# Kernel optimization log

Hardware: AMD Instinct MI355X
Metric: run time of the kernel (lower is better)

The kernel has to match this reference:

```python
import jax, jax.numpy as jnp
import numpy as np

B, T, D, H, C, WIN = 2, 2048, 512, 8, 64, 128
EPS = 1e-6


def _rms_norm(x, w):
    # x: (..., C)
    norm = jax.lax.rsqrt(jnp.mean(x * x, axis=-1, keepdims=True) + EPS)
    return x * norm * w


def _apply_rope(x, cos_p, sin_p):
    # x: (B, H, T, C); cos_p/sin_p: (T, C)
    half = x.shape[-1] // 2
    x1, x2 = x[..., :half], x[..., half:]
    rotated = jnp.concatenate([-x2, x1], axis=-1)
    return x * cos_p + rotated * sin_p


def setup_inputs() -> dict:
    key = jax.random.key(0)
    ks = jax.random.split(key, 5)
    h = jax.random.normal(ks[0], (B, T, D), dtype=jnp.float32)
    # RoPE cache (rotate-half convention): (T_max, head_dim)
    inv_freq = 1.0 / (10000.0 ** (jnp.arange(0, C, 2, dtype=jnp.float32) / C))  # (C/2,)
    pos = jnp.arange(T, dtype=jnp.float32)
    freqs = pos[:, None] * inv_freq[None, :]                      # (T, C/2)
    emb = jnp.concatenate([freqs, freqs], axis=-1)                # (T, C)
    rope_cos = jnp.cos(emb)
    rope_sin = jnp.sin(emb)
    scale = 0.02
    W_q = jax.random.normal(ks[1], (D, H * C), dtype=jnp.float32) * scale
    W_k = jax.random.normal(ks[2], (D, H * C), dtype=jnp.float32) * scale
    W_v = jax.random.normal(ks[3], (D, H * C), dtype=jnp.float32) * scale
    W_o = jax.random.normal(ks[4], (H * C, D), dtype=jnp.float32) * scale
    q_norm_w = jnp.ones((C,), dtype=jnp.float32)
    k_norm_w = jnp.ones((C,), dtype=jnp.float32)
    return {"h": h, "rope_cos": rope_cos, "rope_sin": rope_sin,
            "W_q": W_q, "W_k": W_k, "W_v": W_v, "W_o": W_o,
            "q_norm_w": q_norm_w, "k_norm_w": k_norm_w}


def reference(h, rope_cos, rope_sin, W_q, W_k, W_v, W_o, q_norm_w, k_norm_w):
    Bx, Tx, _ = h.shape
    q = (h @ W_q).reshape(Bx, Tx, H, C)
    k = (h @ W_k).reshape(Bx, Tx, H, C)
    v = (h @ W_v).reshape(Bx, Tx, H, C)
    q = _rms_norm(q, q_norm_w)
    k = _rms_norm(k, k_norm_w)
    positions = jnp.arange(Tx)
    cos_p = rope_cos[positions]   # (T, C)
    sin_p = rope_sin[positions]
    # transpose to (B, H, T, C), apply rope, transpose back handled implicitly
    q = _apply_rope(q.transpose(0, 2, 1, 3), cos_p, sin_p).transpose(0, 2, 1, 3)
    k = _apply_rope(k.transpose(0, 2, 1, 3), cos_p, sin_p).transpose(0, 2, 1, 3)
    i = positions[:, None]
    j = positions[None, :]
    sw_mask = (j <= i) & (j > i - WIN)                # (T, T) banded causal
    logits = jnp.einsum('bthc,bshc->bhts', q, k) / np.sqrt(C).astype(np.float32)
    logits = jnp.where(sw_mask[None, None], logits, jnp.float32(-jnp.inf))
    attn = jax.nn.softmax(logits, axis=-1)
    out = jnp.einsum('bhts,bshc->bthc', attn, v).reshape(Bx, Tx, H * C)
    return out @ W_o
```

## Files before the change

kernel.cpp:

```cpp
#include <hip/hip_runtime.h>
#include <hip/hip_bf16.h>
#include <cmath>

#define Bb 2
#define Tt 2048
#define Dd 512
#define Hh 8
#define Cc 64
#define WINw 128

using u16x8 = __attribute__((ext_vector_type(8))) unsigned short;
using s16x8 = __attribute__((ext_vector_type(8))) short;
using f32x4 = __attribute__((ext_vector_type(4))) float;

__device__ __forceinline__ float bf2f(unsigned short u) {
  union { unsigned int i; float f; } v; v.i = ((unsigned int)u) << 16; return v.f;
}
__device__ __forceinline__ unsigned short f2bf(float f) {
  __hip_bfloat16 b = __float2bfloat16(f);
  return *reinterpret_cast<unsigned short*>(&b);
}

__global__ __launch_bounds__(256) void cvt_f32_bf16(
    const float* __restrict__ src, unsigned short* __restrict__ dst) {
  size_t i = ((size_t)blockIdx.x * 256 + threadIdx.x) * 8;
  const float4* g = (const float4*)&src[i];
  float4 f0 = g[0], f1 = g[1];
  u16x8 o = {f2bf(f0.x), f2bf(f0.y), f2bf(f0.z), f2bf(f0.w),
             f2bf(f1.x), f2bf(f1.y), f2bf(f1.z), f2bf(f1.w)};
  *(u16x8*)&dst[i] = o;
}

__global__ __launch_bounds__(256) void transpose_all(
    const float* __restrict__ s0, const float* __restrict__ s1,
    const float* __restrict__ s2, const float* __restrict__ s3,
    unsigned short* __restrict__ d) {
  __shared__ unsigned short tile[64 * 65];
  const float* srcs[4] = {s0, s1, s2, s3};
  const float* src = srcs[blockIdx.z];
  unsigned short* dst = d + (size_t)blockIdx.z * 512 * 512;
  int n0 = blockIdx.x * 64, k0 = blockIdx.y * 64;
  int tx = threadIdx.x, ty = threadIdx.y;
  #pragma unroll
  for (int i = 0; i < 16; ++i) {
    int k = ty * 16 + i;
    tile[k * 65 + tx] = f2bf(src[(k0 + k) * 512 + n0 + tx]);
  }
  __syncthreads();
  #pragma unroll
  for (int i = 0; i < 16; ++i) {
    int n = ty * 16 + i;
    dst[(n0 + n) * 512 + k0 + tx] = tile[tx * 65 + n];
  }
}

__global__ __launch_bounds__(256) void qkv_fused(
    const unsigned short* __restrict__ Hb,
    const unsigned short* __restrict__ WTall,
    const float* __restrict__ qnw, const float* __restrict__ knw,
    const float* __restrict__ rcos, const float* __restrict__ rsin,
    unsigned short* __restrict__ Qw, unsigned short* __restrict__ Kw,
    unsigned short* __restrict__ Vw) {
  __shared__ alignas(16) unsigned short Al[128 * 72];
  __shared__ alignas(16) unsigned short Bl[128 * 72];
  int m0 = blockIdx.x * 128;
  int n0 = blockIdx.y * 128;
  int tid = threadIdx.x;
  int wave = tid >> 6, lane = tid & 63;
  int ln = lane & 15, qd = lane >> 4;
  int wm = wave >> 1, wn = wave & 1;
  int srow = tid >> 2, scol = (tid & 3) * 16;

  f32x4 acc[4][4];
  #pragma unroll
  for (int mi = 0; mi < 4; ++mi)
    #pragma unroll
    for (int ni = 0; ni < 4; ++ni) acc[mi][ni] = f32x4{0.f, 0.f, 0.f, 0.f};

  for (int k0 = 0; k0 < 512; k0 += 64) {
    #pragma unroll
    for (int p = 0; p < 2; ++p) {
      int row = p * 64 + srow;
      const u16x8* ga = (const u16x8*)&Hb[(size_t)(m0 + row) * 512 + k0 + scol];
      u16x8 a0 = ga[0], a1 = ga[1];
      const u16x8* gb = (const u16x8*)&WTall[(size_t)(n0 + row) * 512 + k0 + scol];
      u16x8 b0 = gb[0], b1 = gb[1];
      *(u16x8*)&Al[row * 72 + scol] = a0;
      *(u16x8*)&Al[row * 72 + scol + 8] = a1;
      *(u16x8*)&Bl[row * 72 + scol] = b0;
      *(u16x8*)&Bl[row * 72 + scol + 8] = b1;
    }
    __syncthreads();
    #pragma unroll
    for (int kk = 0; kk < 64; kk += 32) {
      s16x8 af[4], bfr[4];
      #pragma unroll
      for (int mi = 0; mi < 4; ++mi)
        af[mi] = *(const s16x8*)&Al[(wm * 64 + mi * 16 + ln) * 72 + kk + qd * 8];
      #pragma unroll
      for (int ni = 0; ni < 4; ++ni)
        bfr[ni] = *(const s16x8*)&Bl[(wn * 64 + ni * 16 + ln) * 72 + kk + qd * 8];
      #pragma unroll
      for (int mi = 0; mi < 4; ++mi)
        #pragma unroll
        for (int ni = 0; ni < 4; ++ni)
          acc[mi][ni] = __builtin_amdgcn_mfma_f32_16x16x32_bf16(
              af[mi], bfr[ni], acc[mi][ni], 0, 0, 0);
    }
    __syncthreads();
  }

  int gh = blockIdx.y * 2 + wn;
  int mat = gh >> 3, head = gh & 7;
  unsigned short* Out = (mat == 0) ? Qw : (mat == 1) ? Kw : Vw;
  const float* nw = (mat == 0) ? qnw : knw;
  bool do_rope = (mat < 2);

  #pragma unroll
  for (int mi = 0; mi < 4; ++mi) {
    float vals[4][4];
    #pragma unroll
    for (int ni = 0; ni < 4; ++ni)
      #pragma unroll
      for (int r = 0; r < 4; ++r) vals[ni][r] = acc[mi][ni][r];

    if (do_rope) {
      #pragma unroll
      for (int r = 0; r < 4; ++r) {
        float ss = 0.f;
        #pragma unroll
        for (int ni = 0; ni < 4; ++ni) ss += vals[ni][r] * vals[ni][r];
        ss += __shfl_xor(ss, 1, 64);
        ss += __shfl_xor(ss, 2, 64);
        ss += __shfl_xor(ss, 4, 64);
        ss += __shfl_xor(ss, 8, 64);
        float nrm = rsqrtf(ss * (1.0f / 64.0f) + 1e-6f);
        #pragma unroll
        for (int ni = 0; ni < 4; ++ni) vals[ni][r] *= nrm;
      }
      #pragma unroll
      for (int ni = 0; ni < 4; ++ni) {
        float w = nw[ni * 16 + ln];
        #pragma unroll
        for (int r = 0; r < 4; ++r) vals[ni][r] *= w;
      }
      float res[4][4];
      #pragma unroll
      for (int r = 0; r < 4; ++r) {
        int row = m0 + wm * 64 + mi * 16 + qd * 4 + r;
        int t = row & (Tt - 1);
        #pragma unroll
        for (int ni = 0; ni < 4; ++ni) {
          int c = ni * 16 + ln;
          float cs = rcos[t * 64 + c];
          float sn = rsin[t * 64 + c];
          float part = vals[ni ^ 2][r];
          float rot = (ni < 2) ? -part : part;
          res[ni][r] = vals[ni][r] * cs + rot * sn;
        }
      }
      #pragma unroll
      for (int ni = 0; ni < 4; ++ni)
        #pragma unroll
        for (int r = 0; r < 4; ++r) vals[ni][r] = res[ni][r];
    }

    #pragma unroll
    for (int r = 0; r < 4; ++r) {
      int row = m0 + wm * 64 + mi * 16 + qd * 4 + r;
      int b = row >> 11, t = row & (Tt - 1);
      unsigned short* op = &Out[(((size_t)b * Hh + head) * Tt + t) * 64 + ln];
      #pragma unroll
      for (int ni = 0; ni < 4; ++ni) op[ni * 16] = f2bf(vals[ni][r]);
    }
  }
}

__global__ __launch_bounds__(256) void attn_mfma(
    const unsigned short* __restrict__ Q,
    const unsigned short* __restrict__ K,
    const unsigned short* __restrict__ V,
    unsigned short* __restrict__ AO) {
  __shared__ alignas(16) unsigned short Ql[64 * 72];
  __shared__ alignas(16) unsigned short KP[192 * 72];
  __shared__ alignas(16) unsigned short Vt[64 * 200];

  int tid = threadIdx.x;
  int wave = tid >> 6, lane = tid & 63;
  int ln = lane & 15, qd = lane >> 4;
  int qtile = blockIdx.x, bh = blockIdx.y;
  int t0 = qtile * 64;
  int kb = t0 - 128;

  const unsigned short* Qg = Q + ((size_t)bh * Tt + t0) * 64;
  const unsigned short* Kg = K + (size_t)bh * Tt * 64;
  const unsigned short* Vg = V + (size_t)bh * Tt * 64;

  int srow = tid >> 2;
  int scol = (tid & 3) * 16;

  {
    const u16x8* g = (const u16x8*)&Qg[srow * 64 + scol];
    u16x8 a0 = g[0], a1 = g[1];
    *(u16x8*)&Ql[srow * 72 + scol] = a0;
    *(u16x8*)&Ql[srow * 72 + scol + 8] = a1;
  }
  #pragma unroll
  for (int p = 0; p < 3; ++p) {
    int row = p * 64 + srow;
    int kg = kb + row; if (kg < 0) kg = 0;
    const u16x8* gk = (const u16x8*)&Kg[kg * 64 + scol];
    u16x8 k0 = gk[0], k1 = gk[1];
    const u16x8* gv = (const u16x8*)&Vg[kg * 64 + scol];
    u16x8 v0 = gv[0], v1 = gv[1];
    *(u16x8*)&KP[row * 72 + scol] = k0;
    *(u16x8*)&KP[row * 72 + scol + 8] = k1;
    #pragma unroll
    for (int j = 0; j < 8; ++j) {
      Vt[(scol + j) * 200 + row] = v0[j];
      Vt[(scol + 8 + j) * 200 + row] = v1[j];
    }
  }
  __syncthreads();

  int q0 = wave * 16;
  s16x8 aq0 = *(const s16x8*)&Ql[(q0 + ln) * 72 + qd * 8];
  s16x8 aq1 = *(const s16x8*)&Ql[(q0 + ln) * 72 + 32 + qd * 8];
  f32x4 sf[12];
  #pragma unroll
  for (int nt = 0; nt < 12; ++nt) {
    s16x8 b0 = *(const s16x8*)&KP[(nt * 16 + ln) * 72 + qd * 8];
    s16x8 b1 = *(const s16x8*)&KP[(nt * 16 + ln) * 72 + 32 + qd * 8];
    f32x4 acc = {0.f, 0.f, 0.f, 0.f};
    acc = __builtin_amdgcn_mfma_f32_16x16x32_bf16(aq0, b0, acc, 0, 0, 0);
    acc = __builtin_amdgcn_mfma_f32_16x16x32_bf16(aq1, b1, acc, 0, 0, 0);
    sf[nt] = acc;
  }
  __syncthreads();

  unsigned short* Pl = KP;
  int ok0 = (t0 < 128) ? (128 - t0) : 0;
  #pragma unroll
  for (int r = 0; r < 4; ++r) {
    int lq = q0 + qd * 4 + r;
    float mx = -INFINITY;
    #pragma unroll
    for (int nt = 0; nt < 12; ++nt) {
      int kk = nt * 16 + ln;
      bool valid = (kk > lq) && (kk <= lq + 128) && (kk >= ok0);
      float s = valid ? sf[nt][r] * 0.125f : -INFINITY;
      sf[nt][r] = s;
      mx = fmaxf(mx, s);
    }
    mx = fmaxf(mx, __shfl_xor(mx, 1, 64));
    mx = fmaxf(mx, __shfl_xor(mx, 2, 64));
    mx = fmaxf(mx, __shfl_xor(mx, 4, 64));
    mx = fmaxf(mx, __shfl_xor(mx, 8, 64));
    float sum = 0.f;
    #pragma unroll
    for (int nt = 0; nt < 12; ++nt) {
      float e = __expf(sf[nt][r] - mx);
      sf[nt][r] = e;
      sum += e;
    }
    sum += __shfl_xor(sum, 1, 64);
    sum += __shfl_xor(sum, 2, 64);
    sum += __shfl_xor(sum, 4, 64);
    sum += __shfl_xor(sum, 8, 64);
    float inv = 1.0f / sum;
    #pragma unroll
    for (int nt = 0; nt < 12; ++nt)
      Pl[lq * 200 + nt * 16 + ln] = f2bf(sf[nt][r] * inv);
  }
  __syncthreads();

  f32x4 oa[4] = {f32x4{0,0,0,0}, f32x4{0,0,0,0}, f32x4{0,0,0,0}, f32x4{0,0,0,0}};
  #pragma unroll
  for (int s = 0; s < 6; ++s) {
    s16x8 ap = *(const s16x8*)&Pl[(q0 + ln) * 200 + s * 32 + qd * 8];
    #pragma unroll
    for (int nt = 0; nt < 4; ++nt) {
      s16x8 bv = *(const s16x8*)&Vt[(nt * 16 + ln) * 200 + s * 32 + qd * 8];
      oa[nt] = __builtin_amdgcn_mfma_f32_16x16x32_bf16(ap, bv, oa[nt], 0, 0, 0);
    }
  }

  int b = bh >> 3, h = bh & 7;
  #pragma unroll
  for (int r = 0; r < 4; ++r) {
    int t = t0 + q0 + qd * 4 + r;
    unsigned short* op = &AO[(((size_t)b * Tt + t) * Hh + h) * 64 + ln];
    #pragma unroll
    for (int nt = 0; nt < 4; ++nt) op[nt * 16] = f2bf(oa[nt][r]);
  }
}

__global__ __launch_bounds__(256) void out_gemm128(
    const unsigned short* __restrict__ Am,
    const unsigned short* __restrict__ WT,
    float* __restrict__ Out) {
  __shared__ alignas(16) unsigned short Al[128 * 72];
  __shared__ alignas(16) unsigned short Bl[128 * 72];
  int m0 = blockIdx.x * 128;
  int n0 = blockIdx.y * 128;
  int tid = threadIdx.x;
  int wave = tid >> 6, lane = tid & 63;
  int ln = lane & 15, qd = lane >> 4;
  int wm = wave >> 1, wn = wave & 1;
  int srow = tid >> 2, scol = (tid & 3) * 16;

  f32x4 acc[4][4];
  #pragma unroll
  for (int mi = 0; mi < 4; ++mi)
    #pragma unroll
    for (int ni = 0; ni < 4; ++ni) acc[mi][ni] = f32x4{0.f, 0.f, 0.f, 0.f};

  for (int k0 = 0; k0 < 512; k0 += 64) {
    #pragma unroll
    for (int p = 0; p < 2; ++p) {
      int row = p * 64 + srow;
      const u16x8* ga = (const u16x8*)&Am[(size_t)(m0 + row) * 512 + k0 + scol];
      u16x8 a0 = ga[0], a1 = ga[1];
      const u16x8* gb = (const u16x8*)&WT[(size_t)(n0 + row) * 512 + k0 + scol];
      u16x8 b0 = gb[0], b1 = gb[1];
      *(u16x8*)&Al[row * 72 + scol] = a0;
      *(u16x8*)&Al[row * 72 + scol + 8] = a1;
      *(u16x8*)&Bl[row * 72 + scol] = b0;
      *(u16x8*)&Bl[row * 72 + scol + 8] = b1;
    }
    __syncthreads();
    #pragma unroll
    for (int kk = 0; kk < 64; kk += 32) {
      s16x8 af[4], bfr[4];
      #pragma unroll
      for (int mi = 0; mi < 4; ++mi)
        af[mi] = *(const s16x8*)&Al[(wm * 64 + mi * 16 + ln) * 72 + kk + qd * 8];
      #pragma unroll
      for (int ni = 0; ni < 4; ++ni)
        bfr[ni] = *(const s16x8*)&Bl[(wn * 64 + ni * 16 + ln) * 72 + kk + qd * 8];
      #pragma unroll
      for (int mi = 0; mi < 4; ++mi)
        #pragma unroll
        for (int ni = 0; ni < 4; ++ni)
          acc[mi][ni] = __builtin_amdgcn_mfma_f32_16x16x32_bf16(
              af[mi], bfr[ni], acc[mi][ni], 0, 0, 0);
    }
    __syncthreads();
  }

  #pragma unroll
  for (int mi = 0; mi < 4; ++mi)
    #pragma unroll
    for (int r = 0; r < 4; ++r) {
      int row = m0 + wm * 64 + mi * 16 + qd * 4 + r;
      #pragma unroll
      for (int ni = 0; ni < 4; ++ni)
        Out[(size_t)row * 512 + n0 + wn * 64 + ni * 16 + ln] = acc[mi][ni][r];
    }
}

extern "C" void kernel_launch(void* const* d_in, const int* in_sizes, int n_in,
                              void* d_out, int out_size, void* d_ws, size_t ws_size,
                              hipStream_t stream) {
  const float* h   = (const float*)d_in[0];
  const float* rc  = (const float*)d_in[1];
  const float* rs  = (const float*)d_in[2];
  const float* Wq  = (const float*)d_in[3];
  const float* Wk  = (const float*)d_in[4];
  const float* Wv  = (const float*)d_in[5];
  const float* Wo  = (const float*)d_in[6];
  const float* qnw = (const float*)d_in[7];
  const float* knw = (const float*)d_in[8];

  unsigned short* ws    = (unsigned short*)d_ws;
  unsigned short* WTall = ws;
  unsigned short* WTo   = WTall + 1536 * 512;
  unsigned short* Hb    = WTo + 512 * 512;
  unsigned short* Qw    = Hb + 2097152;
  unsigned short* Kw    = Qw + 2097152;
  unsigned short* Vw    = Kw + 2097152;
  unsigned short* AOw   = Vw + 2097152;

  cvt_f32_bf16<<<1024, 256, 0, stream>>>(h, Hb);
  transpose_all<<<dim3(8, 8, 4), dim3(64, 4), 0, stream>>>(Wq, Wk, Wv, Wo, WTall);

  qkv_fused<<<dim3(32, 12), 256, 0, stream>>>(Hb, WTall, qnw, knw, rc, rs,
                                              Qw, Kw, Vw);

  attn_mfma<<<dim3(32, 16), 256, 0, stream>>>(Qw, Kw, Vw, AOw);

  out_gemm128<<<dim3(32, 4), 256, 0, stream>>>(AOw, WTo, (float*)d_out);
}
```

Before: 116.9 us.

## Merge prep kernels, use direct global-to-LDS loads with XOR swizzle, shrink out-GEMM tile

Folds the h conversion and the weight transposes into one launch, removing a kernel launch. Both GEMMs now stage tiles through global_load_lds straight into an unpadded LDS layout, using an XOR swizzle to avoid bank conflicts, which skips the trip through registers. The output GEMM tile drops from 128 to 64 rows, doubling its block count to fill more CUs. In exchange, the conversion blocks do uneven work relative to the transpose blocks, and the smaller tile reuses less data per block.

```diff
diff --git a/kernel.cpp b/kernel.cpp
--- a/kernel.cpp
+++ b/kernel.cpp
@@ -21,26 +21,36 @@
   return *reinterpret_cast<unsigned short*>(&b);
 }
 
-__global__ __launch_bounds__(256) void cvt_f32_bf16(
-    const float* __restrict__ src, unsigned short* __restrict__ dst) {
-  size_t i = ((size_t)blockIdx.x * 256 + threadIdx.x) * 8;
-  const float4* g = (const float4*)&src[i];
-  float4 f0 = g[0], f1 = g[1];
-  u16x8 o = {f2bf(f0.x), f2bf(f0.y), f2bf(f0.z), f2bf(f0.w),
-             f2bf(f1.x), f2bf(f1.y), f2bf(f1.z), f2bf(f1.w)};
-  *(u16x8*)&dst[i] = o;
-}
-
-__global__ __launch_bounds__(256) void transpose_all(
+#define GLD16(gp, lp)                                                        \
+  __builtin_amdgcn_global_load_lds(                                          \
+      (const __attribute__((address_space(1))) unsigned int*)(gp),           \
+      (__attribute__((address_space(3))) unsigned int*)(lp), 16, 0, 0)
+
+__global__ __launch_bounds__(256) void prep_all(
     const float* __restrict__ s0, const float* __restrict__ s1,
     const float* __restrict__ s2, const float* __restrict__ s3,
-    unsigned short* __restrict__ d) {
+    unsigned short* __restrict__ d,
+    const float* __restrict__ hsrc, unsigned short* __restrict__ hdst) {
+  int tid = threadIdx.x;
+  if (blockIdx.z == 4) {
+    int gid = ((int)blockIdx.y * 8 + blockIdx.x) * 256 + tid;
+    #pragma unroll
+    for (int s = 0; s < 16; ++s) {
+      size_t i = ((size_t)s * 16384 + gid) * 8;
+      const float4* g = (const float4*)&hsrc[i];
+      float4 f0 = g[0], f1 = g[1];
+      u16x8 o = {f2bf(f0.x), f2bf(f0.y), f2bf(f0.z), f2bf(f0.w),
+                 f2bf(f1.x), f2bf(f1.y), f2bf(f1.z), f2bf(f1.w)};
+      *(u16x8*)&hdst[i] = o;
+    }
+    return;
+  }
   __shared__ unsigned short tile[64 * 65];
   const float* srcs[4] = {s0, s1, s2, s3};
   const float* src = srcs[blockIdx.z];
   unsigned short* dst = d + (size_t)blockIdx.z * 512 * 512;
   int n0 = blockIdx.x * 64, k0 = blockIdx.y * 64;
-  int tx = threadIdx.x, ty = threadIdx.y;
+  int tx = tid & 63, ty = tid >> 6;
   #pragma unroll
   for (int i = 0; i < 16; ++i) {
     int k = ty * 16 + i;
@@ -61,15 +71,13 @@
     const float* __restrict__ rcos, const float* __restrict__ rsin,
     unsigned short* __restrict__ Qw, unsigned short* __restrict__ Kw,
     unsigned short* __restrict__ Vw) {
-  __shared__ alignas(16) unsigned short Al[128 * 72];
-  __shared__ alignas(16) unsigned short Bl[128 * 72];
-  int m0 = blockIdx.x * 128;
-  int n0 = blockIdx.y * 128;
+  __shared__ alignas(16) unsigned short Al[128 * 64];
+  __shared__ alignas(16) unsigned short Bl[128 * 64];
   int tid = threadIdx.x;
   int wave = tid >> 6, lane = tid & 63;
   int ln = lane & 15, qd = lane >> 4;
   int wm = wave >> 1, wn = wave & 1;
-  int srow = tid >> 2, scol = (tid & 3) * 16;
+  int m0 = blockIdx.x * 128, n0 = blockIdx.y * 128;
 
   f32x4 acc[4][4];
   #pragma unroll
@@ -79,27 +87,32 @@
 
   for (int k0 = 0; k0 < 512; k0 += 64) {
     #pragma unroll
-    for (int p = 0; p < 2; ++p) {
-      int row = p * 64 + srow;
-      const u16x8* ga = (const u16x8*)&Hb[(size_t)(m0 + row) * 512 + k0 + scol];
-      u16x8 a0 = ga[0], a1 = ga[1];
-      const u16x8* gb = (const u16x8*)&WTall[(size_t)(n0 + row) * 512 + k0 + scol];
-      u16x8 b0 = gb[0], b1 = gb[1];
-      *(u16x8*)&Al[row * 72 + scol] = a0;
-      *(u16x8*)&Al[row * 72 + scol + 8] = a1;
-      *(u16x8*)&Bl[row * 72 + scol] = b0;
-      *(u16x8*)&Bl[row * 72 + scol + 8] = b1;
+    for (int s = 0; s < 4; ++s) {
+      int q = s * 4 + wave;
+      int L = q * 64 + lane;
+      int row = L >> 3;
+      int cb = (L & 7) ^ (row & 7);
+      const unsigned short* ga = &Hb[(size_t)(m0 + row) * 512 + k0 + cb * 8];
+      GLD16(ga, (char*)Al + q * 1024);
+      const unsigned short* gb = &WTall[(size_t)(n0 + row) * 512 + k0 + cb * 8];
+      GLD16(gb, (char*)Bl + q * 1024);
     }
     __syncthreads();
     #pragma unroll
-    for (int kk = 0; kk < 64; kk += 32) {
+    for (int half = 0; half < 2; ++half) {
       s16x8 af[4], bfr[4];
       #pragma unroll
-      for (int mi = 0; mi < 4; ++mi)
-        af[mi] = *(const s16x8*)&Al[(wm * 64 + mi * 16 + ln) * 72 + kk + qd * 8];
-      #pragma unroll
-      for (int ni = 0; ni < 4; ++ni)
-        bfr[ni] = *(const s16x8*)&Bl[(wn * 64 + ni * 16 + ln) * 72 + kk + qd * 8];
+      for (int mi = 0; mi < 4; ++mi) {
+        int ar = wm * 64 + mi * 16 + ln;
+        int cbp = (qd + half * 4) ^ (ar & 7);
+        af[mi] = *(const s16x8*)((const char*)Al + ar * 128 + cbp * 16);
+      }
+      #pragma unroll
+      for (int ni = 0; ni < 4; ++ni) {
+        int br = wn * 64 + ni * 16 + ln;
+        int cbp = (qd + half * 4) ^ (br & 7);
+        bfr[ni] = *(const s16x8*)((const char*)Bl + br * 128 + cbp * 16);
+      }
       #pragma unroll
       for (int mi = 0; mi < 4; ++mi)
         #pragma unroll
@@ -295,51 +308,61 @@
   }
 }
 
-__global__ __launch_bounds__(256) void out_gemm128(
+__global__ __launch_bounds__(256) void out_gemm(
     const unsigned short* __restrict__ Am,
     const unsigned short* __restrict__ WT,
     float* __restrict__ Out) {
-  __shared__ alignas(16) unsigned short Al[128 * 72];
-  __shared__ alignas(16) unsigned short Bl[128 * 72];
-  int m0 = blockIdx.x * 128;
-  int n0 = blockIdx.y * 128;
+  __shared__ alignas(16) unsigned short Al[64 * 64];
+  __shared__ alignas(16) unsigned short Bl[128 * 64];
   int tid = threadIdx.x;
   int wave = tid >> 6, lane = tid & 63;
   int ln = lane & 15, qd = lane >> 4;
   int wm = wave >> 1, wn = wave & 1;
-  int srow = tid >> 2, scol = (tid & 3) * 16;
-
-  f32x4 acc[4][4];
-  #pragma unroll
-  for (int mi = 0; mi < 4; ++mi)
+  int m0 = blockIdx.x * 64, n0 = blockIdx.y * 128;
+
+  f32x4 acc[2][4];
+  #pragma unroll
+  for (int mi = 0; mi < 2; ++mi)
     #pragma unroll
     for (int ni = 0; ni < 4; ++ni) acc[mi][ni] = f32x4{0.f, 0.f, 0.f, 0.f};
 
   for (int k0 = 0; k0 < 512; k0 += 64) {
     #pragma unroll
-    for (int p = 0; p < 2; ++p) {
-      int row = p * 64 + srow;
-      const u16x8* ga = (const u16x8*)&Am[(size_t)(m0 + row) * 512 + k0 + scol];
-      u16x8 a0 = ga[0], a1 = ga[1];
-      const u16x8* gb = (const u16x8*)&WT[(size_t)(n0 + row) * 512 + k0 + scol];
-      u16x8 b0 = gb[0], b1 = gb[1];
-      *(u16x8*)&Al[row * 72 + scol] = a0;
-      *(u16x8*)&Al[row * 72 + scol + 8] = a1;
-      *(u16x8*)&Bl[row * 72 + scol] = b0;
-      *(u16x8*)&Bl[row * 72 + scol + 8] = b1;
+    for (int s = 0; s < 2; ++s) {
+      int q = s * 4 + wave;
+      int L = q * 64 + lane;
+      int row = L >> 3;
+      int cb = (L & 7) ^ (row & 7);
+      const unsigned short* ga = &Am[(size_t)(m0 + row) * 512 + k0 + cb * 8];
+      GLD16(ga, (char*)Al + q * 1024);
+    }
+    #pragma unroll
+    for (int s = 0; s < 4; ++s) {
+      int q = s * 4 + wave;
+      int L = q * 64 + lane;
+      int row = L >> 3;
+      int cb = (L & 7) ^ (row & 7);
+      const unsigned short* gb = &WT[(size_t)(n0 + row) * 512 + k0 + cb * 8];
+      GLD16(gb, (char*)Bl + q * 1024);
     }
     __syncthreads();
     #pragma unroll
-    for (int kk = 0; kk < 64; kk += 32) {
-      s16x8 af[4], bfr[4];
-      #pragma unroll
-      for (int mi = 0; mi < 4; ++mi)
-        af[mi] = *(const s16x8*)&Al[(wm * 64 + mi * 16 + ln) * 72 + kk + qd * 8];
-      #pragma unroll
-      for (int ni = 0; ni < 4; ++ni)
-        bfr[ni] = *(const s16x8*)&Bl[(wn * 64 + ni * 16 + ln) * 72 + kk + qd * 8];
-      #pragma unroll
-      for (int mi = 0; mi < 4; ++mi)
+    for (int half = 0; half < 2; ++half) {
+      s16x8 af[2], bfr[4];
+      #pragma unroll
+      for (int mi = 0; mi < 2; ++mi) {
+        int ar = wm * 32 + mi * 16 + ln;
+        int cbp = (qd + half * 4) ^ (ar & 7);
+        af[mi] = *(const s16x8*)((const char*)Al + ar * 128 + cbp * 16);
+      }
+      #pragma unroll
+      for (int ni = 0; ni < 4; ++ni) {
+        int br = wn * 64 + ni * 16 + ln;
+        int cbp = (qd + half * 4) ^ (br & 7);
+        bfr[ni] = *(const s16x8*)((const char*)Bl + br * 128 + cbp * 16);
+      }
+      #pragma unroll
+      for (int mi = 0; mi < 2; ++mi)
         #pragma unroll
         for (int ni = 0; ni < 4; ++ni)
           acc[mi][ni] = __builtin_amdgcn_mfma_f32_16x16x32_bf16(
@@ -349,10 +372,10 @@
   }
 
   #pragma unroll
-  for (int mi = 0; mi < 4; ++mi)
+  for (int mi = 0; mi < 2; ++mi)
     #pragma unroll
     for (int r = 0; r < 4; ++r) {
-      int row = m0 + wm * 64 + mi * 16 + qd * 4 + r;
+      int row = m0 + wm * 32 + mi * 16 + qd * 4 + r;
       #pragma unroll
       for (int ni = 0; ni < 4; ++ni)
         Out[(size_t)row * 512 + n0 + wn * 64 + ni * 16 + ln] = acc[mi][ni][r];
@@ -381,13 +404,12 @@
   unsigned short* Vw    = Kw + 2097152;
   unsigned short* AOw   = Vw + 2097152;
 
-  cvt_f32_bf16<<<1024, 256, 0, stream>>>(h, Hb);
-  transpose_all<<<dim3(8, 8, 4), dim3(64, 4), 0, stream>>>(Wq, Wk, Wv, Wo, WTall);
+  prep_all<<<dim3(8, 8, 5), 256, 0, stream>>>(Wq, Wk, Wv, Wo, WTall, h, Hb);
 
   qkv_fused<<<dim3(32, 12), 256, 0, stream>>>(Hb, WTall, qnw, knw, rc, rs,
                                               Qw, Kw, Vw);
 
   attn_mfma<<<dim3(32, 16), 256, 0, stream>>>(Qw, Kw, Vw, AOw);
 
-  out_gemm128<<<dim3(32, 4), 256, 0, stream>>>(AOw, WTo, (float*)d_out);
-}
+  out_gemm<<<dim3(64, 4), 256, 0, stream>>>(AOw, WTo, (float*)d_out);
+}
```

Result: faster. 114.1 us (-2.4%).
